# Kernel tuning notes

Measured on AMD Instinct MI355X. Metric: run time of the kernel, lower is better.

## Reference

```python
import jax, jax.numpy as jnp
import numpy as np

B, D, N, L, M = 32, 64, 128, 192, 32  # batch, channels, nodes, seq_len, modes
LH = L // 2 + 1  # rfft length = 97


def setup_inputs() -> dict:
    key = jax.random.key(0)
    k1, k2, k3 = jax.random.split(key, 3)
    scale = 1.0 / (D * D)  # 1/(in_channels*out_channels)
    q = jax.random.normal(k1, (B, D, N, L), dtype=jnp.float32)
    w_real = scale * jax.random.uniform(k2, (N, D, D, M), dtype=jnp.float32)
    w_imag = scale * jax.random.uniform(k3, (N, D, D, M), dtype=jnp.float32)
    return {"q": q, "w_real": w_real, "w_imag": w_imag}


def reference(q, w_real, w_imag):
    # mode_select_method='lowest' -> index = [0, 1, ..., M-1] (static)
    index = np.arange(M)
    x = jnp.transpose(q, (0, 2, 1, 3))            # [B, N, D, L]
    x_ft = jnp.fft.rfft(x, axis=-1)               # [B, N, D, LH] complex64
    w = (w_real + 1j * w_imag).astype(jnp.complex64)  # [N, D, D, M]
    sel = x_ft[..., index]                        # gather selected modes [B, N, D, M]
    # fused replacement of the per-mode einsum loop: one batched complex einsum
    out_sel = jnp.einsum('bnim,niom->bnom', sel, w)  # [B, N, D, M]
    out_ft = jnp.zeros((B, N, D, LH), dtype=jnp.complex64).at[..., :M].set(out_sel)
    out = jnp.fft.irfft(out_ft, n=L, axis=-1)     # [B, N, D, L] real
    return jnp.transpose(out, (0, 2, 1, 3))       # [B, D, N, L]
```

## Files before the change

kernel.cpp:

```cpp
#include <hip/hip_runtime.h>
#include <stdint.h>


typedef __attribute__((ext_vector_type(8))) short short8;
typedef __attribute__((ext_vector_type(4))) float f32x4;
typedef __attribute__((ext_vector_type(4))) unsigned short u16x4;

__device__ __forceinline__ unsigned short f2bf(float f) {
  union { float fv; uint32_t u; } v; v.fv = f;
  uint32_t u = v.u;
  u += 0x7fffu + ((u >> 16) & 1u);
  return (unsigned short)(u >> 16);
}

__device__ __forceinline__ f32x4 zero4() { f32x4 z; z[0]=0.f; z[1]=0.f; z[2]=0.f; z[3]=0.f; return z; }

#define TWO_PI_OVER_L (6.283185307179586f / 192.0f)

__global__ __launch_bounds__(512, 1)
void k1n_dft(const float* __restrict__ q, unsigned short* __restrict__ Xp) {
  extern __shared__ char smem[];
  float* qS = (float*)smem;
  unsigned short* Fb = (unsigned short*)(smem + 100352);
  unsigned short* XE = (unsigned short*)(smem + 125952);
  const int t = threadIdx.x, lane = t & 63, w = t >> 6;
  const int l15 = lane & 15, g = lane >> 4;
  const int bid = blockIdx.x;
  const int ih = bid & 1, bq = (bid >> 1) & 7, nq = bid >> 4;
  const int b0 = bq * 4;

  for (int idx = t; idx < 64 * 192; idx += 512) {
    int cat = idx / 192, l = idx - cat * 192;
    int m = cat >> 1;
    int r = (m * l) % 192;
    float ang = (float)r * TWO_PI_OVER_L;
    float v = (cat & 1) ? -__sinf(ang) : __cosf(ang);
    Fb[cat * 200 + l] = f2bf(v);
  }

  for (int nn = 0; nn < 4; ++nn) {
    const int n = nq * 4 + nn;

    float4 stg[12];
#pragma unroll
    for (int j = 0; j < 12; ++j) {
      int fq = (w * 12 + j) * 64 + lane;
      int row = fq / 48;
      int qd = fq - row * 48;
      int b = b0 + (row >> 5);
      int i = ih * 32 + (row & 31);
      stg[j] = *(const float4*)(q + ((size_t)((b * 64 + i) * 128 + n)) * 192 + qd * 4);
    }
#pragma unroll
    for (int j = 0; j < 12; ++j) {
      int fq = (w * 12 + j) * 64 + lane;
      int row = fq / 48;
      int qd = fq - row * 48;
      *(float4*)(qS + row * 196 + qd * 4) = stg[j];
    }
    __syncthreads();

    f32x4 acc[4];
#pragma unroll
    for (int a = 0; a < 4; ++a) acc[a] = zero4();

    const int row = w * 16 + l15;
#pragma unroll
    for (int kc = 0; kc < 6; ++kc) {
      f32x4 lo = *(const f32x4*)(qS + row * 196 + kc * 32 + g * 8);
      f32x4 hi = *(const f32x4*)(qS + row * 196 + kc * 32 + g * 8 + 4);
      short8 A;
      A[0] = (short)f2bf(lo[0]); A[1] = (short)f2bf(lo[1]);
      A[2] = (short)f2bf(lo[2]); A[3] = (short)f2bf(lo[3]);
      A[4] = (short)f2bf(hi[0]); A[5] = (short)f2bf(hi[1]);
      A[6] = (short)f2bf(hi[2]); A[7] = (short)f2bf(hi[3]);
#pragma unroll
      for (int nt = 0; nt < 4; ++nt) {
        short8 Bf = *(const short8*)(Fb + (nt * 16 + l15) * 200 + kc * 32 + g * 8);
        acc[nt] = __builtin_amdgcn_mfma_f32_16x16x32_bf16(A, Bf, acc[nt], 0, 0, 0);
      }
    }

    const int b_loc = w >> 1, i_base = (w & 1) * 16 + g * 4;
#pragma unroll
    for (int nt = 0; nt < 4; ++nt) {
      int cat = nt * 16 + l15;
      f32x4 v = acc[nt];
#pragma unroll
      for (int r = 0; r < 4; ++r)
        XE[cat * 128 + b_loc * 32 + i_base + r] = f2bf(v[r]);
    }
    __syncthreads();

#pragma unroll
    for (int cc2 = 0; cc2 < 2; ++cc2) {
      int ch = cc2 * 512 + t;
      int m = ch >> 5, c = (ch >> 4) & 1, g2 = (ch >> 2) & 3, dl = ch & 3;
      short8 v = *(const short8*)(XE + (2 * m + c) * 128 + dl * 32 + g2 * 8);
      int lanep = g2 * 16 + (b0 & 15) + dl;
      int off = n * 131072 + ((((m * 2 + c) * 2 + ih) * 2 + (b0 >> 4)) * 64 + lanep) * 8;
      *(short8*)(Xp + off) = v;
    }
    __syncthreads();
  }
}

#define K2_OSTRIDE 34
#define K2_ISTRIDE 546
#define K2_CSTRIDE 34944
__global__ __launch_bounds__(512, 2)
void k2f_mix(const float* __restrict__ wr, const float* __restrict__ wi,
             const unsigned short* __restrict__ Xp, unsigned short* __restrict__ Yp) {
  extern __shared__ char smem[];
  unsigned short* T = (unsigned short*)smem;
  const int t = threadIdx.x, lane = t & 63, w = t >> 6;
  const int n = blockIdx.x >> 2, oq = blockIdx.x & 3;
  const int ol = lane & 15, il0 = (lane >> 4) * 8;

#pragma unroll
  for (int j = 0; j < 32; ++j) {
    int f = j * 512 + t;
    int mg = f & 7, o = (f >> 3) & 15, i = (f >> 7) & 63, c = (f >> 13) & 1;
    const float* src = (c ? wi : wr) + ((n * 64 + i) * 64 + oq * 16 + o) * 32 + mg * 4;
    float4 v = *(const float4*)src;
    u16x4 h; h[0] = f2bf(v.x); h[1] = f2bf(v.y); h[2] = f2bf(v.z); h[3] = f2bf(v.w);
    *(u16x4*)(T + c * K2_CSTRIDE + i * K2_ISTRIDE + o * K2_OSTRIDE + mg * 4) = h;
  }
  __syncthreads();

#pragma unroll
  for (int mm = 0; mm < 4; ++mm) {
    int m = w * 4 + mm;
    f32x4 acc[2][2];
#pragma unroll
    for (int a = 0; a < 2; ++a)
#pragma unroll
      for (int b2 = 0; b2 < 2; ++b2) acc[a][b2] = zero4();

#pragma unroll
    for (int ic = 0; ic < 2; ++ic) {
      const unsigned short* xb = Xp + n * 131072 + m * 4096 + ic * 1024 + lane * 8;
      short8 Ar0 = *(const short8*)(xb);
      short8 Ar1 = *(const short8*)(xb + 512);
      short8 Ai0 = *(const short8*)(xb + 2048);
      short8 Ai1 = *(const short8*)(xb + 2048 + 512);

      const unsigned short* tb = T + (ic * 32 + il0) * K2_ISTRIDE + ol * K2_OSTRIDE + m;
      short8 Br, Bi, nBi;
#pragma unroll
      for (int e = 0; e < 8; ++e) {
        Br[e] = (short)tb[e * K2_ISTRIDE];
        Bi[e] = (short)tb[K2_CSTRIDE + e * K2_ISTRIDE];
        nBi[e] = Bi[e] ^ (short)0x8000;
      }

      acc[0][0] = __builtin_amdgcn_mfma_f32_16x16x32_bf16(Ar0, Br,  acc[0][0], 0, 0, 0);
      acc[0][0] = __builtin_amdgcn_mfma_f32_16x16x32_bf16(Ai0, nBi, acc[0][0], 0, 0, 0);
      acc[0][1] = __builtin_amdgcn_mfma_f32_16x16x32_bf16(Ar1, Br,  acc[0][1], 0, 0, 0);
      acc[0][1] = __builtin_amdgcn_mfma_f32_16x16x32_bf16(Ai1, nBi, acc[0][1], 0, 0, 0);
      acc[1][0] = __builtin_amdgcn_mfma_f32_16x16x32_bf16(Ar0, Bi,  acc[1][0], 0, 0, 0);
      acc[1][0] = __builtin_amdgcn_mfma_f32_16x16x32_bf16(Ai0, Br,  acc[1][0], 0, 0, 0);
      acc[1][1] = __builtin_amdgcn_mfma_f32_16x16x32_bf16(Ar1, Bi,  acc[1][1], 0, 0, 0);
      acc[1][1] = __builtin_amdgcn_mfma_f32_16x16x32_bf16(Ai1, Br,  acc[1][1], 0, 0, 0);
    }

    const int g = lane >> 4;
#pragma unroll
    for (int cc = 0; cc < 2; ++cc) {
      int cat = 2 * m + cc;
#pragma unroll
      for (int Mt = 0; Mt < 2; ++Mt) {
        f32x4 v = acc[cc][Mt];
#pragma unroll
        for (int r = 0; r < 4; ++r) {
          int b = Mt * 16 + g * 4 + r;
          Yp[((n * 32 + b) * 64 + cat) * 64 + oq * 16 + ol] = f2bf(v[r]);
        }
      }
    }
  }
}

__global__ __launch_bounds__(256, 4)
void k3_idft(const unsigned short* __restrict__ Yp, float* __restrict__ out) {
  extern __shared__ char smem[];
  unsigned short* Yl = (unsigned short*)smem;
  float* ol = (float*)(smem + 8192);
  const int t = threadIdx.x, lane = t & 63, w = t >> 6;
  const int n = blockIdx.x & 127, b = blockIdx.x >> 7;

  const unsigned short* ysrc = Yp + (n * 32 + b) * 4096;
#pragma unroll
  for (int j = 0; j < 2; ++j) {
    int f = j * 256 + t;
    *(short8*)(Yl + f * 8) = *(const short8*)(ysrc + f * 8);
  }

  short8 Af[3][2];
#pragma unroll
  for (int jm = 0; jm < 3; ++jm) {
    int Mt = w + 4 * jm;
    int lt = Mt * 16 + (lane & 15);
#pragma unroll
    for (int kc = 0; kc < 2; ++kc) {
#pragma unroll
      for (int e = 0; e < 8; ++e) {
        int cat = kc * 32 + (lane >> 4) * 8 + e;
        int m = cat >> 1;
        int r = (m * lt) % 192;
        float ang = (float)r * TWO_PI_OVER_L;
        float coef = (m == 0) ? (1.0f / 192.0f) : (2.0f / 192.0f);
        float v = ((cat & 1) ? -__sinf(ang) : __cosf(ang)) * coef;
        Af[jm][kc][e] = (short)f2bf(v);
      }
    }
  }
  __syncthreads();

  f32x4 acc[3][4];
#pragma unroll
  for (int a = 0; a < 3; ++a)
#pragma unroll
    for (int bq = 0; bq < 4; ++bq) acc[a][bq] = zero4();

#pragma unroll
  for (int kc = 0; kc < 2; ++kc) {
    short8 Bf[4];
#pragma unroll
    for (int nt = 0; nt < 4; ++nt)
#pragma unroll
      for (int e = 0; e < 8; ++e) {
        int cat = kc * 32 + (lane >> 4) * 8 + e;
        Bf[nt][e] = (short)Yl[cat * 64 + nt * 16 + (lane & 15)];
      }
#pragma unroll
    for (int jm = 0; jm < 3; ++jm)
#pragma unroll
      for (int nt = 0; nt < 4; ++nt)
        acc[jm][nt] = __builtin_amdgcn_mfma_f32_16x16x32_bf16(Af[jm][kc], Bf[nt], acc[jm][nt], 0, 0, 0);
  }

#pragma unroll
  for (int jm = 0; jm < 3; ++jm) {
    int Mt = w + 4 * jm;
    int l0 = Mt * 16 + (lane >> 4) * 4;
#pragma unroll
    for (int nt = 0; nt < 4; ++nt) {
      int o = nt * 16 + (lane & 15);
      int lp = l0 ^ ((o & 7) << 2);
      *(f32x4*)(ol + o * 192 + lp) = acc[jm][nt];
    }
  }
  __syncthreads();

  float* dst = out + (b * 64 * 128 + n) * 192;
#pragma unroll
  for (int j = 0; j < 12; ++j) {
    int f = j * 256 + t;
    int o = f / 48, g2 = f - o * 48;
    int lp = g2 * 4;
    int l = lp ^ ((o & 7) << 2);
    f32x4 v = *(const f32x4*)(ol + o * 192 + lp);
    *(f32x4*)(dst + o * (128 * 192) + l) = v;
  }
}

extern "C" void kernel_launch(void* const* d_in, const int* in_sizes, int n_in,
                              void* d_out, int out_size, void* d_ws, size_t ws_size,
                              hipStream_t stream) {
  const float* q  = (const float*)d_in[0];
  const float* wr = (const float*)d_in[1];
  const float* wi = (const float*)d_in[2];
  float* out = (float*)d_out;

  unsigned short* Xp = (unsigned short*)d_ws;
  unsigned short* Yp = Xp + 16777216;

  hipFuncSetAttribute((const void*)k1n_dft, hipFuncAttributeMaxDynamicSharedMemorySize, 142336);
  hipFuncSetAttribute((const void*)k2f_mix, hipFuncAttributeMaxDynamicSharedMemorySize, 139776);
  hipFuncSetAttribute((const void*)k3_idft, hipFuncAttributeMaxDynamicSharedMemorySize, 57344);

  k1n_dft<<<dim3(512), dim3(512), 142336, stream>>>(q, Xp);
  k2f_mix<<<dim3(512), dim3(512), 139776, stream>>>(wr, wi, Xp, Yp);
  k3_idft<<<dim3(4096), dim3(256), 57344, stream>>>(Yp, out);
}
```

Baseline: 193.1 us.

## Split DFT into streaming GEMM plus pack kernel, halve mix-kernel LDS

The forward DFT kernel is split in two. A high-occupancy kernel reads q rows directly from global memory and writes contiguous bf16 spectra to an extra workspace buffer. A separate pack kernel then transposes them into the MFMA-friendly layout. The twiddle table is now built from a cosine lookup rather than per-element sin/cos. The mixing kernel stages weights in two input-channel halves, which halves its LDS and allows more blocks per CU. The cost is an extra launch and an extra round trip of intermediate data through global memory.

```diff
diff --git a/kernel.cpp b/kernel.cpp
--- a/kernel.cpp
+++ b/kernel.cpp
@@ -17,160 +17,168 @@
 
 #define TWO_PI_OVER_L (6.283185307179586f / 192.0f)
 
-__global__ __launch_bounds__(512, 1)
-void k1n_dft(const float* __restrict__ q, unsigned short* __restrict__ Xp) {
-  extern __shared__ char smem[];
-  float* qS = (float*)smem;
-  unsigned short* Fb = (unsigned short*)(smem + 100352);
-  unsigned short* XE = (unsigned short*)(smem + 125952);
+__global__ __launch_bounds__(256, 4)
+void k1s_dft(const float* __restrict__ q, unsigned short* __restrict__ X1) {
+  extern __shared__ char smem[];
+  float* costab = (float*)smem;
+  unsigned short* Fb = (unsigned short*)(smem + 768);
   const int t = threadIdx.x, lane = t & 63, w = t >> 6;
   const int l15 = lane & 15, g = lane >> 4;
-  const int bid = blockIdx.x;
-  const int ih = bid & 1, bq = (bid >> 1) & 7, nq = bid >> 4;
-  const int b0 = bq * 4;
-
-  for (int idx = t; idx < 64 * 192; idx += 512) {
+
+  for (int j = t; j < 192; j += 256)
+    costab[j] = __cosf((float)j * TWO_PI_OVER_L);
+  __syncthreads();
+  for (int idx = t; idx < 64 * 192; idx += 256) {
     int cat = idx / 192, l = idx - cat * 192;
     int m = cat >> 1;
     int r = (m * l) % 192;
-    float ang = (float)r * TWO_PI_OVER_L;
-    float v = (cat & 1) ? -__sinf(ang) : __cosf(ang);
-    Fb[cat * 200 + l] = f2bf(v);
-  }
-
-  for (int nn = 0; nn < 4; ++nn) {
-    const int n = nq * 4 + nn;
-
-    float4 stg[12];
-#pragma unroll
-    for (int j = 0; j < 12; ++j) {
-      int fq = (w * 12 + j) * 64 + lane;
-      int row = fq / 48;
-      int qd = fq - row * 48;
-      int b = b0 + (row >> 5);
-      int i = ih * 32 + (row & 31);
-      stg[j] = *(const float4*)(q + ((size_t)((b * 64 + i) * 128 + n)) * 192 + qd * 4);
-    }
-#pragma unroll
-    for (int j = 0; j < 12; ++j) {
-      int fq = (w * 12 + j) * 64 + lane;
-      int row = fq / 48;
-      int qd = fq - row * 48;
-      *(float4*)(qS + row * 196 + qd * 4) = stg[j];
-    }
-    __syncthreads();
-
+    if (cat & 1) { r += 48; if (r >= 192) r -= 192; }
+    Fb[cat * 200 + l] = f2bf(costab[r]);
+  }
+  __syncthreads();
+
+  for (int rr = 0; rr < 2; ++rr) {
+    const int row0 = blockIdx.x * 128 + w * 32 + rr * 16;
     f32x4 acc[4];
 #pragma unroll
     for (int a = 0; a < 4; ++a) acc[a] = zero4();
 
-    const int row = w * 16 + l15;
+    const float* qrow = q + (size_t)(row0 + l15) * 192;
 #pragma unroll
     for (int kc = 0; kc < 6; ++kc) {
-      f32x4 lo = *(const f32x4*)(qS + row * 196 + kc * 32 + g * 8);
-      f32x4 hi = *(const f32x4*)(qS + row * 196 + kc * 32 + g * 8 + 4);
+      float4 lo = *(const float4*)(qrow + kc * 32 + g * 8);
+      float4 hi = *(const float4*)(qrow + kc * 32 + g * 8 + 4);
       short8 A;
-      A[0] = (short)f2bf(lo[0]); A[1] = (short)f2bf(lo[1]);
-      A[2] = (short)f2bf(lo[2]); A[3] = (short)f2bf(lo[3]);
-      A[4] = (short)f2bf(hi[0]); A[5] = (short)f2bf(hi[1]);
-      A[6] = (short)f2bf(hi[2]); A[7] = (short)f2bf(hi[3]);
+      A[0] = (short)f2bf(lo.x); A[1] = (short)f2bf(lo.y);
+      A[2] = (short)f2bf(lo.z); A[3] = (short)f2bf(lo.w);
+      A[4] = (short)f2bf(hi.x); A[5] = (short)f2bf(hi.y);
+      A[6] = (short)f2bf(hi.z); A[7] = (short)f2bf(hi.w);
 #pragma unroll
       for (int nt = 0; nt < 4; ++nt) {
         short8 Bf = *(const short8*)(Fb + (nt * 16 + l15) * 200 + kc * 32 + g * 8);
         acc[nt] = __builtin_amdgcn_mfma_f32_16x16x32_bf16(A, Bf, acc[nt], 0, 0, 0);
       }
     }
-
-    const int b_loc = w >> 1, i_base = (w & 1) * 16 + g * 4;
 #pragma unroll
     for (int nt = 0; nt < 4; ++nt) {
-      int cat = nt * 16 + l15;
       f32x4 v = acc[nt];
 #pragma unroll
       for (int r = 0; r < 4; ++r)
-        XE[cat * 128 + b_loc * 32 + i_base + r] = f2bf(v[r]);
-    }
-    __syncthreads();
-
-#pragma unroll
-    for (int cc2 = 0; cc2 < 2; ++cc2) {
-      int ch = cc2 * 512 + t;
-      int m = ch >> 5, c = (ch >> 4) & 1, g2 = (ch >> 2) & 3, dl = ch & 3;
-      short8 v = *(const short8*)(XE + (2 * m + c) * 128 + dl * 32 + g2 * 8);
-      int lanep = g2 * 16 + (b0 & 15) + dl;
-      int off = n * 131072 + ((((m * 2 + c) * 2 + ih) * 2 + (b0 >> 4)) * 64 + lanep) * 8;
-      *(short8*)(Xp + off) = v;
-    }
-    __syncthreads();
-  }
-}
-
-#define K2_OSTRIDE 34
-#define K2_ISTRIDE 546
-#define K2_CSTRIDE 34944
-__global__ __launch_bounds__(512, 2)
-void k2f_mix(const float* __restrict__ wr, const float* __restrict__ wi,
+        X1[(size_t)(row0 + g * 4 + r) * 64 + nt * 16 + l15] = f2bf(v[r]);
+    }
+  }
+}
+
+__global__ __launch_bounds__(256, 2)
+void k1t_pack(const unsigned short* __restrict__ X1, unsigned short* __restrict__ Xp) {
+  extern __shared__ char smem[];
+  unsigned short* T = (unsigned short*)smem;
+  const int t = threadIdx.x;
+  const int bid = blockIdx.x;
+  const int ih = bid & 1, Mt2 = (bid >> 1) & 1, n = bid >> 2;
+  const int i5 = t >> 3, c8 = t & 7;
+
+  short8 rbuf[16];
+#pragma unroll
+  for (int b = 0; b < 16; ++b) {
+    size_t row = (size_t)(((Mt2 * 16 + b) * 64) + ih * 32 + i5) * 128 + n;
+    rbuf[b] = *(const short8*)(X1 + row * 64 + c8 * 8);
+  }
+#pragma unroll
+  for (int b = 0; b < 16; ++b)
+    *(short8*)(T + (i5 * 16 + b) * 66 + c8 * 8) = rbuf[b];
+  __syncthreads();
+
+#pragma unroll
+  for (int j = 0; j < 16; ++j) {
+    int f = j * 256 + t;
+    int cat = f >> 6, s = f & 63;
+    int b15 = s & 15, gg = s >> 4;
+    short8 v;
+#pragma unroll
+    for (int e = 0; e < 8; ++e)
+      v[e] = (short)T[((gg * 8 + e) * 16 + b15) * 66 + cat];
+    *(short8*)(Xp + n * 131072 + cat * 2048 + ih * 1024 + Mt2 * 512 + s * 8) = v;
+  }
+}
+
+__global__ __launch_bounds__(512, 4)
+void k2h_mix(const float* __restrict__ wr, const float* __restrict__ wi,
              const unsigned short* __restrict__ Xp, unsigned short* __restrict__ Yp) {
   extern __shared__ char smem[];
   unsigned short* T = (unsigned short*)smem;
   const int t = threadIdx.x, lane = t & 63, w = t >> 6;
   const int n = blockIdx.x >> 2, oq = blockIdx.x & 3;
-  const int ol = lane & 15, il0 = (lane >> 4) * 8;
-
-#pragma unroll
-  for (int j = 0; j < 32; ++j) {
-    int f = j * 512 + t;
-    int mg = f & 7, o = (f >> 3) & 15, i = (f >> 7) & 63, c = (f >> 13) & 1;
-    const float* src = (c ? wi : wr) + ((n * 64 + i) * 64 + oq * 16 + o) * 32 + mg * 4;
-    float4 v = *(const float4*)src;
-    u16x4 h; h[0] = f2bf(v.x); h[1] = f2bf(v.y); h[2] = f2bf(v.z); h[3] = f2bf(v.w);
-    *(u16x4*)(T + c * K2_CSTRIDE + i * K2_ISTRIDE + o * K2_OSTRIDE + mg * 4) = h;
-  }
-  __syncthreads();
-
-#pragma unroll
-  for (int mm = 0; mm < 4; ++mm) {
-    int m = w * 4 + mm;
-    f32x4 acc[2][2];
-#pragma unroll
-    for (int a = 0; a < 2; ++a)
-#pragma unroll
-      for (int b2 = 0; b2 < 2; ++b2) acc[a][b2] = zero4();
-
-#pragma unroll
-    for (int ic = 0; ic < 2; ++ic) {
+  const int ol = lane & 15, il0 = (lane >> 4) * 8, g = lane >> 4;
+
+  f32x4 acc[4][2][2];
+#pragma unroll
+  for (int a = 0; a < 4; ++a)
+#pragma unroll
+    for (int c2 = 0; c2 < 2; ++c2)
+#pragma unroll
+      for (int b2 = 0; b2 < 2; ++b2) acc[a][c2][b2] = zero4();
+
+  for (int ic = 0; ic < 2; ++ic) {
+    if (ic) __syncthreads();
+#pragma unroll
+    for (int jb = 0; jb < 4; ++jb) {
+      float4 s[4];
+#pragma unroll
+      for (int k = 0; k < 4; ++k) {
+        int f = (jb * 4 + k) * 512 + t;
+        int mg = f & 7, o = (f >> 3) & 15, i = (f >> 7) & 31, c = (f >> 12) & 1;
+        s[k] = *(const float4*)((c ? wi : wr) +
+                ((n * 64 + ic * 32 + i) * 64 + oq * 16 + o) * 32 + mg * 4);
+      }
+#pragma unroll
+      for (int k = 0; k < 4; ++k) {
+        int f = (jb * 4 + k) * 512 + t;
+        int mg = f & 7, o = (f >> 3) & 15, i = (f >> 7) & 31, c = (f >> 12) & 1;
+        u16x4 h; h[0] = f2bf(s[k].x); h[1] = f2bf(s[k].y); h[2] = f2bf(s[k].z); h[3] = f2bf(s[k].w);
+        *(u16x4*)(T + c * 17472 + i * 546 + o * 34 + mg * 4) = h;
+      }
+    }
+    __syncthreads();
+
+#pragma unroll
+    for (int mm = 0; mm < 4; ++mm) {
+      int m = w * 4 + mm;
       const unsigned short* xb = Xp + n * 131072 + m * 4096 + ic * 1024 + lane * 8;
       short8 Ar0 = *(const short8*)(xb);
       short8 Ar1 = *(const short8*)(xb + 512);
       short8 Ai0 = *(const short8*)(xb + 2048);
       short8 Ai1 = *(const short8*)(xb + 2048 + 512);
 
-      const unsigned short* tb = T + (ic * 32 + il0) * K2_ISTRIDE + ol * K2_OSTRIDE + m;
+      const unsigned short* tb = T + il0 * 546 + ol * 34 + m;
       short8 Br, Bi, nBi;
 #pragma unroll
       for (int e = 0; e < 8; ++e) {
-        Br[e] = (short)tb[e * K2_ISTRIDE];
-        Bi[e] = (short)tb[K2_CSTRIDE + e * K2_ISTRIDE];
+        Br[e] = (short)tb[e * 546];
+        Bi[e] = (short)tb[17472 + e * 546];
         nBi[e] = Bi[e] ^ (short)0x8000;
       }
 
-      acc[0][0] = __builtin_amdgcn_mfma_f32_16x16x32_bf16(Ar0, Br,  acc[0][0], 0, 0, 0);
-      acc[0][0] = __builtin_amdgcn_mfma_f32_16x16x32_bf16(Ai0, nBi, acc[0][0], 0, 0, 0);
-      acc[0][1] = __builtin_amdgcn_mfma_f32_16x16x32_bf16(Ar1, Br,  acc[0][1], 0, 0, 0);
-      acc[0][1] = __builtin_amdgcn_mfma_f32_16x16x32_bf16(Ai1, nBi, acc[0][1], 0, 0, 0);
-      acc[1][0] = __builtin_amdgcn_mfma_f32_16x16x32_bf16(Ar0, Bi,  acc[1][0], 0, 0, 0);
-      acc[1][0] = __builtin_amdgcn_mfma_f32_16x16x32_bf16(Ai0, Br,  acc[1][0], 0, 0, 0);
-      acc[1][1] = __builtin_amdgcn_mfma_f32_16x16x32_bf16(Ar1, Bi,  acc[1][1], 0, 0, 0);
-      acc[1][1] = __builtin_amdgcn_mfma_f32_16x16x32_bf16(Ai1, Br,  acc[1][1], 0, 0, 0);
-    }
-
-    const int g = lane >> 4;
+      acc[mm][0][0] = __builtin_amdgcn_mfma_f32_16x16x32_bf16(Ar0, Br,  acc[mm][0][0], 0, 0, 0);
+      acc[mm][0][0] = __builtin_amdgcn_mfma_f32_16x16x32_bf16(Ai0, nBi, acc[mm][0][0], 0, 0, 0);
+      acc[mm][0][1] = __builtin_amdgcn_mfma_f32_16x16x32_bf16(Ar1, Br,  acc[mm][0][1], 0, 0, 0);
+      acc[mm][0][1] = __builtin_amdgcn_mfma_f32_16x16x32_bf16(Ai1, nBi, acc[mm][0][1], 0, 0, 0);
+      acc[mm][1][0] = __builtin_amdgcn_mfma_f32_16x16x32_bf16(Ar0, Bi,  acc[mm][1][0], 0, 0, 0);
+      acc[mm][1][0] = __builtin_amdgcn_mfma_f32_16x16x32_bf16(Ai0, Br,  acc[mm][1][0], 0, 0, 0);
+      acc[mm][1][1] = __builtin_amdgcn_mfma_f32_16x16x32_bf16(Ar1, Bi,  acc[mm][1][1], 0, 0, 0);
+      acc[mm][1][1] = __builtin_amdgcn_mfma_f32_16x16x32_bf16(Ai1, Br,  acc[mm][1][1], 0, 0, 0);
+    }
+  }
+
+#pragma unroll
+  for (int mm = 0; mm < 4; ++mm) {
+    int m = w * 4 + mm;
 #pragma unroll
     for (int cc = 0; cc < 2; ++cc) {
       int cat = 2 * m + cc;
 #pragma unroll
       for (int Mt = 0; Mt < 2; ++Mt) {
-        f32x4 v = acc[cc][Mt];
+        f32x4 v = acc[mm][cc][Mt];
 #pragma unroll
         for (int r = 0; r < 4; ++r) {
           int b = Mt * 16 + g * 4 + r;
@@ -275,12 +283,15 @@
 
   unsigned short* Xp = (unsigned short*)d_ws;
   unsigned short* Yp = Xp + 16777216;
-
-  hipFuncSetAttribute((const void*)k1n_dft, hipFuncAttributeMaxDynamicSharedMemorySize, 142336);
-  hipFuncSetAttribute((const void*)k2f_mix, hipFuncAttributeMaxDynamicSharedMemorySize, 139776);
+  unsigned short* X1 = Xp + 33554432;
+
+  hipFuncSetAttribute((const void*)k1s_dft, hipFuncAttributeMaxDynamicSharedMemorySize, 26368);
+  hipFuncSetAttribute((const void*)k1t_pack, hipFuncAttributeMaxDynamicSharedMemorySize, 67584);
+  hipFuncSetAttribute((const void*)k2h_mix, hipFuncAttributeMaxDynamicSharedMemorySize, 69888);
   hipFuncSetAttribute((const void*)k3_idft, hipFuncAttributeMaxDynamicSharedMemorySize, 57344);
 
-  k1n_dft<<<dim3(512), dim3(512), 142336, stream>>>(q, Xp);
-  k2f_mix<<<dim3(512), dim3(512), 139776, stream>>>(wr, wi, Xp, Yp);
+  k1s_dft<<<dim3(2048), dim3(256), 26368, stream>>>(q, X1);
+  k1t_pack<<<dim3(512), dim3(256), 67584, stream>>>(X1, Xp);
+  k2h_mix<<<dim3(512), dim3(512), 69888, stream>>>(wr, wi, Xp, Yp);
   k3_idft<<<dim3(4096), dim3(256), 57344, stream>>>(Yp, out);
 }
```

Result: slower. 218.3 us (+13.0%).

## Double-buffer bf16 q tiles in DFT kernel and reblock Y layout between mix and iDFT

Applied to the files above, without the earlier changes.

The DFT kernel now converts q to bf16 when staging it into shared memory and double-buffers the tiles. The global loads for the next node are issued before the current MFMA loop, which removes one barrier per iteration and halves the q shared-memory footprint. The XE stride is padded to cut bank conflicts. The mix kernel writes Y in per-(n, oq) blocks so each thread stores contiguous pairs, and the iDFT kernel gathers from that layout into a padded LDS tile. The extra complexity is higher register pressure from holding the staged loads across the compute loop.

```diff
diff --git a/kernel.cpp b/kernel.cpp
--- a/kernel.cpp
+++ b/kernel.cpp
@@ -18,11 +18,12 @@
 #define TWO_PI_OVER_L (6.283185307179586f / 192.0f)
 
 __global__ __launch_bounds__(512, 1)
-void k1n_dft(const float* __restrict__ q, unsigned short* __restrict__ Xp) {
+void k1d_dft(const float* __restrict__ q, unsigned short* __restrict__ Xp) {
   extern __shared__ char smem[];
-  float* qS = (float*)smem;
-  unsigned short* Fb = (unsigned short*)(smem + 100352);
-  unsigned short* XE = (unsigned short*)(smem + 125952);
+  unsigned short* qB0 = (unsigned short*)smem;
+  unsigned short* qB1 = (unsigned short*)(smem + 51200);
+  unsigned short* Fb  = (unsigned short*)(smem + 102400);
+  unsigned short* XE  = (unsigned short*)(smem + 128000);
   const int t = threadIdx.x, lane = t & 63, w = t >> 6;
   const int l15 = lane & 15, g = lane >> 4;
   const int bid = blockIdx.x;
@@ -38,42 +39,55 @@
     Fb[cat * 200 + l] = f2bf(v);
   }
 
+  int srow[12], sqd[12];
+#pragma unroll
+  for (int j = 0; j < 12; ++j) {
+    int fq = (w * 12 + j) * 64 + lane;
+    srow[j] = fq / 48;
+    sqd[j] = fq - srow[j] * 48;
+  }
+  size_t qoff[12];
+#pragma unroll
+  for (int j = 0; j < 12; ++j) {
+    int row = srow[j];
+    int b = b0 + (row >> 5), i = ih * 32 + (row & 31);
+    qoff[j] = ((size_t)((b * 64 + i) * 128)) * 192 + sqd[j] * 4;
+  }
+  __syncthreads();
+
+  float4 stg[12];
+  {
+    const int n = nq * 4;
+#pragma unroll
+    for (int j = 0; j < 12; ++j)
+      stg[j] = *(const float4*)(q + qoff[j] + (size_t)n * 192);
+#pragma unroll
+    for (int j = 0; j < 12; ++j) {
+      u16x4 h; h[0] = f2bf(stg[j].x); h[1] = f2bf(stg[j].y);
+      h[2] = f2bf(stg[j].z); h[3] = f2bf(stg[j].w);
+      *(u16x4*)(qB0 + srow[j] * 200 + sqd[j] * 4) = h;
+    }
+  }
+  __syncthreads();
+
   for (int nn = 0; nn < 4; ++nn) {
     const int n = nq * 4 + nn;
-
-    float4 stg[12];
-#pragma unroll
-    for (int j = 0; j < 12; ++j) {
-      int fq = (w * 12 + j) * 64 + lane;
-      int row = fq / 48;
-      int qd = fq - row * 48;
-      int b = b0 + (row >> 5);
-      int i = ih * 32 + (row & 31);
-      stg[j] = *(const float4*)(q + ((size_t)((b * 64 + i) * 128 + n)) * 192 + qd * 4);
-    }
-#pragma unroll
-    for (int j = 0; j < 12; ++j) {
-      int fq = (w * 12 + j) * 64 + lane;
-      int row = fq / 48;
-      int qd = fq - row * 48;
-      *(float4*)(qS + row * 196 + qd * 4) = stg[j];
-    }
-    __syncthreads();
+    unsigned short* cur = (nn & 1) ? qB1 : qB0;
+    unsigned short* nxt = (nn & 1) ? qB0 : qB1;
+
+    if (nn < 3) {
+#pragma unroll
+      for (int j = 0; j < 12; ++j)
+        stg[j] = *(const float4*)(q + qoff[j] + (size_t)(n + 1) * 192);
+    }
 
     f32x4 acc[4];
 #pragma unroll
     for (int a = 0; a < 4; ++a) acc[a] = zero4();
-
     const int row = w * 16 + l15;
 #pragma unroll
     for (int kc = 0; kc < 6; ++kc) {
-      f32x4 lo = *(const f32x4*)(qS + row * 196 + kc * 32 + g * 8);
-      f32x4 hi = *(const f32x4*)(qS + row * 196 + kc * 32 + g * 8 + 4);
-      short8 A;
-      A[0] = (short)f2bf(lo[0]); A[1] = (short)f2bf(lo[1]);
-      A[2] = (short)f2bf(lo[2]); A[3] = (short)f2bf(lo[3]);
-      A[4] = (short)f2bf(hi[0]); A[5] = (short)f2bf(hi[1]);
-      A[6] = (short)f2bf(hi[2]); A[7] = (short)f2bf(hi[3]);
+      short8 A = *(const short8*)(cur + row * 200 + kc * 32 + g * 8);
 #pragma unroll
       for (int nt = 0; nt < 4; ++nt) {
         short8 Bf = *(const short8*)(Fb + (nt * 16 + l15) * 200 + kc * 32 + g * 8);
@@ -81,6 +95,16 @@
       }
     }
 
+    if (nn < 3) {
+#pragma unroll
+      for (int j = 0; j < 12; ++j) {
+        u16x4 h; h[0] = f2bf(stg[j].x); h[1] = f2bf(stg[j].y);
+        h[2] = f2bf(stg[j].z); h[3] = f2bf(stg[j].w);
+        *(u16x4*)(nxt + srow[j] * 200 + sqd[j] * 4) = h;
+      }
+    }
+    __syncthreads();
+
     const int b_loc = w >> 1, i_base = (w & 1) * 16 + g * 4;
 #pragma unroll
     for (int nt = 0; nt < 4; ++nt) {
@@ -88,7 +112,7 @@
       f32x4 v = acc[nt];
 #pragma unroll
       for (int r = 0; r < 4; ++r)
-        XE[cat * 128 + b_loc * 32 + i_base + r] = f2bf(v[r]);
+        XE[cat * 132 + b_loc * 32 + i_base + r] = f2bf(v[r]);
     }
     __syncthreads();
 
@@ -96,12 +120,11 @@
     for (int cc2 = 0; cc2 < 2; ++cc2) {
       int ch = cc2 * 512 + t;
       int m = ch >> 5, c = (ch >> 4) & 1, g2 = (ch >> 2) & 3, dl = ch & 3;
-      short8 v = *(const short8*)(XE + (2 * m + c) * 128 + dl * 32 + g2 * 8);
+      short8 v = *(const short8*)(XE + (2 * m + c) * 132 + dl * 32 + g2 * 8);
       int lanep = g2 * 16 + (b0 & 15) + dl;
       int off = n * 131072 + ((((m * 2 + c) * 2 + ih) * 2 + (b0 >> 4)) * 64 + lanep) * 8;
       *(short8*)(Xp + off) = v;
     }
-    __syncthreads();
   }
 }
 
@@ -109,7 +132,7 @@
 #define K2_ISTRIDE 546
 #define K2_CSTRIDE 34944
 __global__ __launch_bounds__(512, 2)
-void k2f_mix(const float* __restrict__ wr, const float* __restrict__ wi,
+void k2i_mix(const float* __restrict__ wr, const float* __restrict__ wi,
              const unsigned short* __restrict__ Xp, unsigned short* __restrict__ Yp) {
   extern __shared__ char smem[];
   unsigned short* T = (unsigned short*)smem;
@@ -127,6 +150,8 @@
     *(u16x4*)(T + c * K2_CSTRIDE + i * K2_ISTRIDE + o * K2_OSTRIDE + mg * 4) = h;
   }
   __syncthreads();
+
+  unsigned short* yblk = Yp + (n * 4 + oq) * 32768;
 
 #pragma unroll
   for (int mm = 0; mm < 4; ++mm) {
@@ -166,18 +191,14 @@
 
     const int g = lane >> 4;
 #pragma unroll
-    for (int cc = 0; cc < 2; ++cc) {
-      int cat = 2 * m + cc;
-#pragma unroll
-      for (int Mt = 0; Mt < 2; ++Mt) {
-        f32x4 v = acc[cc][Mt];
-#pragma unroll
-        for (int r = 0; r < 4; ++r) {
-          int b = Mt * 16 + g * 4 + r;
-          Yp[((n * 32 + b) * 64 + cat) * 64 + oq * 16 + ol] = f2bf(v[r]);
-        }
-      }
-    }
+    for (int Mt = 0; Mt < 2; ++Mt)
+#pragma unroll
+      for (int r = 0; r < 4; ++r) {
+        int b = Mt * 16 + g * 4 + r;
+        unsigned short* yb = yblk + b * 1024 + (2 * m) * 16 + ol;
+        yb[0]  = f2bf(acc[0][Mt][r]);
+        yb[16] = f2bf(acc[1][Mt][r]);
+      }
   }
 }
 
@@ -185,15 +206,19 @@
 void k3_idft(const unsigned short* __restrict__ Yp, float* __restrict__ out) {
   extern __shared__ char smem[];
   unsigned short* Yl = (unsigned short*)smem;
-  float* ol = (float*)(smem + 8192);
+  float* ol = (float*)(smem + 8448);
   const int t = threadIdx.x, lane = t & 63, w = t >> 6;
   const int n = blockIdx.x & 127, b = blockIdx.x >> 7;
 
-  const unsigned short* ysrc = Yp + (n * 32 + b) * 4096;
+  const unsigned short* ysrc = Yp + (n * 4 * 32 + b) * 1024;
 #pragma unroll
   for (int j = 0; j < 2; ++j) {
     int f = j * 256 + t;
-    *(short8*)(Yl + f * 8) = *(const short8*)(ysrc + f * 8);
+    int og = f & 1, cat = (f >> 1) & 63, oq = f >> 7;
+    short8 v = *(const short8*)(ysrc + oq * 32768 + cat * 16 + og * 8);
+    unsigned int* d = (unsigned int*)(Yl + cat * 66 + oq * 16 + og * 8);
+    union { short8 s; unsigned int u[4]; } uu; uu.s = v;
+    d[0] = uu.u[0]; d[1] = uu.u[1]; d[2] = uu.u[2]; d[3] = uu.u[3];
   }
 
   short8 Af[3][2];
@@ -231,7 +256,7 @@
 #pragma unroll
       for (int e = 0; e < 8; ++e) {
         int cat = kc * 32 + (lane >> 4) * 8 + e;
-        Bf[nt][e] = (short)Yl[cat * 64 + nt * 16 + (lane & 15)];
+        Bf[nt][e] = (short)Yl[cat * 66 + nt * 16 + (lane & 15)];
       }
 #pragma unroll
     for (int jm = 0; jm < 3; ++jm)
@@ -276,11 +301,11 @@
   unsigned short* Xp = (unsigned short*)d_ws;
   unsigned short* Yp = Xp + 16777216;
 
-  hipFuncSetAttribute((const void*)k1n_dft, hipFuncAttributeMaxDynamicSharedMemorySize, 142336);
-  hipFuncSetAttribute((const void*)k2f_mix, hipFuncAttributeMaxDynamicSharedMemorySize, 139776);
-  hipFuncSetAttribute((const void*)k3_idft, hipFuncAttributeMaxDynamicSharedMemorySize, 57344);
-
-  k1n_dft<<<dim3(512), dim3(512), 142336, stream>>>(q, Xp);
-  k2f_mix<<<dim3(512), dim3(512), 139776, stream>>>(wr, wi, Xp, Yp);
-  k3_idft<<<dim3(4096), dim3(256), 57344, stream>>>(Yp, out);
-}
+  hipFuncSetAttribute((const void*)k1d_dft, hipFuncAttributeMaxDynamicSharedMemorySize, 144896);
+  hipFuncSetAttribute((const void*)k2i_mix, hipFuncAttributeMaxDynamicSharedMemorySize, 139776);
+  hipFuncSetAttribute((const void*)k3_idft, hipFuncAttributeMaxDynamicSharedMemorySize, 57600);
+
+  k1d_dft<<<dim3(512), dim3(512), 144896, stream>>>(q, Xp);
+  k2i_mix<<<dim3(512), dim3(512), 139776, stream>>>(wr, wi, Xp, Yp);
+  k3_idft<<<dim3(4096), dim3(256), 57600, stream>>>(Yp, out);
+}
```

Measured after the change: 173.8 us. -10.0%, faster.
